# Kernel optimization log

Measured on AMD Instinct MI355X. Metric: run time of the kernel, lower is better.

The kernel has to match this reference:

```python
import jax, jax.numpy as jnp
import numpy as np


def setup_inputs() -> dict:
    key = jax.random.key(0)
    ks = jax.random.split(key, 7)
    N = 262144
    Ka, La = 8, 8
    Kb, Lb, Mb = 8, 8, 4
    Kc, Lc, Mc = 8, 8, 4
    return {
        "x": jax.random.normal(ks[0], (N, 2), dtype=jnp.float32),
        "a_real": 0.001 * jax.random.normal(ks[1], (Ka, La), dtype=jnp.float32),
        "a_imag": 0.001 * jax.random.normal(ks[2], (Ka, La), dtype=jnp.float32),
        "b_real": 0.001 * jax.random.normal(ks[3], (Kb, Lb, Mb), dtype=jnp.float32),
        "b_imag": 0.001 * jax.random.normal(ks[4], (Kb, Lb, Mb), dtype=jnp.float32),
        "c_real": 0.001 * jax.random.normal(ks[5], (Kc, Lc, Mc), dtype=jnp.float32),
        "c_imag": 0.001 * jax.random.normal(ks[6], (Kc, Lc, Mc), dtype=jnp.float32),
    }


def _gmp(x, a_real, a_imag, b_real, b_imag, c_real, c_imag):
    # x: (N,2) real I/Q -> complex signal (iq_handler equivalent)
    xc = (x[:, 0] + 1j * x[:, 1]).astype(jnp.complex64)
    a = (a_real + 1j * a_imag).astype(jnp.complex64)   # (Ka,La)
    b = (b_real + 1j * b_imag).astype(jnp.complex64)   # (Kb,Lb,Mb)
    c = (c_real + 1j * c_imag).astype(jnp.complex64)   # (Kc,Lc,Mc)
    N = xc.shape[0]
    Ka, La = a.shape
    Kb, Lb, Mb = b.shape
    Kc, Lc, Mc = c.shape
    n = jnp.arange(N)

    # ---- aligned term (a): delayed taps, power series in |x[n-l]| ----
    idx_La = jnp.clip(n[None, :] - jnp.arange(La)[:, None], 0, N - 1)   # (La,N)
    x_La = xc[idx_La]                                                   # (La,N)
    pow_a = jnp.abs(x_La)[..., None] ** jnp.arange(Ka, dtype=jnp.float32)  # (La,N,Ka)
    term_a = jnp.einsum('kl,ln,lnk->n', a, x_La, pow_a)

    # ---- lagging cross-term (b): envelope delayed by extra m >= 0 ----
    idx_Lb = jnp.clip(n[None, :] - jnp.arange(Lb)[:, None], 0, N - 1)   # (Lb,N)
    x_Lb = xc[idx_Lb]                                                   # (Lb,N)
    idx_Mb = jnp.clip(n[None, None, :] - jnp.arange(Lb)[:, None, None]
                      - jnp.arange(Mb)[None, :, None], 0, N - 1)        # (Lb,Mb,N)
    x_Mb = xc[idx_Mb]                                                   # (Lb,Mb,N)
    pow_b = jnp.abs(x_Mb)[..., None] ** jnp.arange(Kb, dtype=jnp.float32)  # (Lb,Mb,N,Kb)
    term_b = jnp.einsum('klm,ln,lmnk->n', b, x_Lb, pow_b)

    # ---- leading cross-term (c): envelope advanced by m >= 0 ----
    idx_Lc = jnp.clip(n[None, :] - jnp.arange(Lc)[:, None], 0, N - 1)   # (Lc,N)
    x_Lc = xc[idx_Lc]                                                   # (Lc,N)
    idx_Mc = jnp.clip(n[None, None, :] - jnp.arange(Lc)[:, None, None]
                      + jnp.arange(Mc)[None, :, None], 0, N - 1)        # (Lc,Mc,N)
    x_Mc = xc[idx_Mc]                                                   # (Lc,Mc,N)
    pow_c = jnp.abs(x_Mc)[..., None] ** jnp.arange(Kc, dtype=jnp.float32)  # (Lc,Mc,N,Kc)
    term_c = jnp.einsum('klm,ln,lmnk->n', c, x_Lc, pow_c)

    y = term_a + term_b + term_c                                        # (N,) complex
    return jnp.stack([y.real, y.imag], axis=-1)                         # back to I/Q (N,2)


def reference(x, a_real, a_imag, b_real, b_imag, c_real, c_imag):
    return _gmp(x, a_real, a_imag, b_real, b_imag, c_real, c_imag)
```

## Files before the change

kernel.cpp:

```cpp
#include <hip/hip_runtime.h>
#include <type_traits>

typedef float v2f __attribute__((ext_vector_type(2)));

template <typename T>
using cptr = T __attribute__((address_space(4)))*;

constexpr int BLOCK = 256;
constexpr int SPB = 128;
constexpr int HALO_LO = 10;
constexpr int HALO_HI = 3;
constexpr int SIG = SPB + HALO_LO + HALO_HI;

template<int I, int N, typename F>
__device__ __forceinline__ void unroll_for(F&& f) {
    if constexpr (I < N) {
        f(std::integral_constant<int, I>{});
        unroll_for<I + 1, N>(static_cast<F&&>(f));
    }
}

__global__ void prefold_kernel(
    const float* __restrict__ a_re, const float* __restrict__ a_im,
    const float* __restrict__ b_re, const float* __restrict__ b_im,
    const float* __restrict__ c_re, const float* __restrict__ c_im,
    float* __restrict__ w)
{
    int idx = threadIdx.x;
    if (idx >= 448) return;
    int l = idx / 56;
    int rem = idx - l * 56;
    int s = rem >> 3;
    int k = rem & 7;
    int akl = k * 8 + l;
    float re, im;
    if (s == 0) {
        re = a_re[akl] + b_re[akl * 4] + c_re[akl * 4];
        im = a_im[akl] + b_im[akl * 4] + c_im[akl * 4];
    } else if (s <= 3) {
        re = b_re[akl * 4 + s];
        im = b_im[akl * 4 + s];
    } else {
        re = c_re[akl * 4 + (s - 3)];
        im = c_im[akl * 4 + (s - 3)];
    }
    w[idx * 2]     = re;
    w[idx * 2 + 1] = im;
}

__global__ __launch_bounds__(BLOCK, 8) void gmp_kernel(
    const float* __restrict__ x,
    const float* __restrict__ wbuf,
    float* __restrict__ out, int N)
{
    __shared__ float2 sx[SIG];
    __shared__ float sab[SIG];
    __shared__ float2 part[4][SPB];

    const int t = threadIdx.x;
    const int n0 = blockIdx.x * SPB;

    const float2* x2 = (const float2*)x;
    if (t < SIG) {
        int g = n0 - HALO_LO + t;
        g = max(0, min(N - 1, g));
        float2 v = x2[g];
        sx[t] = v;
        sab[t] = __builtin_amdgcn_sqrtf(fmaf(v.x, v.x, v.y * v.y));
    }
    __syncthreads();

    const int s2 = t & 63;
    const int wv = __builtin_amdgcn_readfirstlane(t >> 6);
    auto cw = (cptr<const float>)(unsigned long long)(wbuf + wv * 224);

    const int rb = 2 * s2 + 6 - 2 * wv;
    float rv[9];
    unroll_for<0, 9>([&](auto I) { rv[I.value] = sab[rb + I.value]; });
    float xvr[3], xvi[3];
    unroll_for<0, 3>([&](auto I) {
        float2 v = sx[rb + 3 + I.value];
        xvr[I.value] = v.x;
        xvi[I.value] = v.y;
    });

    float y0r = 0.f, y0i = 0.f, y1r = 0.f, y1i = 0.f;

    unroll_for<0, 2>([&](auto LL) {
        constexpr int ll = LL.value;
        v2f S0 = {0.f, 0.f}, S1 = {0.f, 0.f};
        unroll_for<0, 7>([&](auto Sc) {
            constexpr int s = Sc.value;
            constexpr int d = (s == 0) ? 0 : ((s <= 3) ? -s : (s - 3));
            constexpr int off = ll * 112 + s * 16;
            float cre[8], cim[8];
            unroll_for<0, 8>([&](auto K) {
                cre[K.value] = cw[off + 2 * K.value];
                cim[K.value] = cw[off + 2 * K.value + 1];
            });
            const float r0 = rv[4 - ll + d];
            const float r1 = rv[5 - ll + d];
            const v2f rr0 = {r0, r0};
            const v2f rr1 = {r1, r1};
            v2f acc0 = {cre[7], cim[7]};
            v2f acc1 = acc0;
            unroll_for<0, 7>([&](auto Kc) {
                constexpr int k = 6 - Kc.value;
                const v2f wk = {cre[k], cim[k]};
                acc0 = __builtin_elementwise_fma(acc0, rr0, wk);
                acc1 = __builtin_elementwise_fma(acc1, rr1, wk);
            });
            S0 += acc0;
            S1 += acc1;
        });
        {
            const float xre = xvr[1 - ll], xim = xvi[1 - ll];
            y0r = fmaf(xre, S0.x, fmaf(-xim, S0.y, y0r));
            y0i = fmaf(xre, S0.y, fmaf( xim, S0.x, y0i));
        }
        {
            const float xre = xvr[2 - ll], xim = xvi[2 - ll];
            y1r = fmaf(xre, S1.x, fmaf(-xim, S1.y, y1r));
            y1i = fmaf(xre, S1.y, fmaf( xim, S1.x, y1i));
        }
    });

    part[wv][2 * s2]     = make_float2(y0r, y0i);
    part[wv][2 * s2 + 1] = make_float2(y1r, y1i);
    __syncthreads();

    if (t < SPB) {
        float2 p0 = part[0][t];
        float2 p1 = part[1][t];
        float2 p2 = part[2][t];
        float2 p3 = part[3][t];
        float2 r;
        r.x = (p0.x + p1.x) + (p2.x + p3.x);
        r.y = (p0.y + p1.y) + (p2.y + p3.y);
        const int n = n0 + t;
        if (n < N) ((float2*)out)[n] = r;
    }
}

extern "C" void kernel_launch(void* const* d_in, const int* in_sizes, int n_in,
                              void* d_out, int out_size, void* d_ws, size_t ws_size,
                              hipStream_t stream) {
    const float* x    = (const float*)d_in[0];
    const float* a_re = (const float*)d_in[1];
    const float* a_im = (const float*)d_in[2];
    const float* b_re = (const float*)d_in[3];
    const float* b_im = (const float*)d_in[4];
    const float* c_re = (const float*)d_in[5];
    const float* c_im = (const float*)d_in[6];
    float* out = (float*)d_out;
    float* w   = (float*)d_ws;

    int N = in_sizes[0] / 2;
    prefold_kernel<<<1, 448, 0, stream>>>(a_re, a_im, b_re, b_im, c_re, c_im, w);
    int grid = (N + SPB - 1) / SPB;
    gmp_kernel<<<grid, BLOCK, 0, stream>>>(x, w, out, N);
}
```

Baseline: 15.36 us.

## Fuse coefficient prefold into main kernel and stage weights in LDS

Removes the separate single-block prefold launch. Every block now folds the a/b/c coefficients itself into a shared-memory buffer, and the main loop reads the weights as float2 from LDS instead of through scalar constant-address loads. This drops one kernel launch and the dependency between the two kernels. In exchange, every block repeats the gather of about 1.3K coefficient floats, and the weight reads move from scalar registers and the SGPR path to vector LDS loads, which may add LDS pressure and VGPR use. The occupancy hint of 8 in launch_bounds is also removed.

Result: faster. 14.04 us (-8.6%).

```diff
diff --git a/kernel.cpp b/kernel.cpp
--- a/kernel.cpp
+++ b/kernel.cpp
@@ -2,9 +2,6 @@
 #include <type_traits>
 
 typedef float v2f __attribute__((ext_vector_type(2)));
-
-template <typename T>
-using cptr = T __attribute__((address_space(4)))*;
 
 constexpr int BLOCK = 256;
 constexpr int SPB = 128;
@@ -20,42 +17,17 @@
     }
 }
 
-__global__ void prefold_kernel(
+__global__ __launch_bounds__(BLOCK) void gmp_kernel(
+    const float* __restrict__ x,
     const float* __restrict__ a_re, const float* __restrict__ a_im,
     const float* __restrict__ b_re, const float* __restrict__ b_im,
     const float* __restrict__ c_re, const float* __restrict__ c_im,
-    float* __restrict__ w)
-{
-    int idx = threadIdx.x;
-    if (idx >= 448) return;
-    int l = idx / 56;
-    int rem = idx - l * 56;
-    int s = rem >> 3;
-    int k = rem & 7;
-    int akl = k * 8 + l;
-    float re, im;
-    if (s == 0) {
-        re = a_re[akl] + b_re[akl * 4] + c_re[akl * 4];
-        im = a_im[akl] + b_im[akl * 4] + c_im[akl * 4];
-    } else if (s <= 3) {
-        re = b_re[akl * 4 + s];
-        im = b_im[akl * 4 + s];
-    } else {
-        re = c_re[akl * 4 + (s - 3)];
-        im = c_im[akl * 4 + (s - 3)];
-    }
-    w[idx * 2]     = re;
-    w[idx * 2 + 1] = im;
-}
-
-__global__ __launch_bounds__(BLOCK, 8) void gmp_kernel(
-    const float* __restrict__ x,
-    const float* __restrict__ wbuf,
     float* __restrict__ out, int N)
 {
     __shared__ float2 sx[SIG];
     __shared__ float sab[SIG];
     __shared__ float2 part[4][SPB];
+    __shared__ __align__(16) float wlds[896];
 
     const int t = threadIdx.x;
     const int n0 = blockIdx.x * SPB;
@@ -68,11 +40,32 @@
         sx[t] = v;
         sab[t] = __builtin_amdgcn_sqrtf(fmaf(v.x, v.x, v.y * v.y));
     }
+
+    for (int idx = t; idx < 448; idx += BLOCK) {
+        int l = idx / 56;
+        int rem = idx - l * 56;
+        int s = rem >> 3;
+        int k = rem & 7;
+        int akl = k * 8 + l;
+        float re, im;
+        if (s == 0) {
+            re = a_re[akl] + b_re[akl * 4] + c_re[akl * 4];
+            im = a_im[akl] + b_im[akl * 4] + c_im[akl * 4];
+        } else if (s <= 3) {
+            re = b_re[akl * 4 + s];
+            im = b_im[akl * 4 + s];
+        } else {
+            re = c_re[akl * 4 + (s - 3)];
+            im = c_im[akl * 4 + (s - 3)];
+        }
+        wlds[idx * 2]     = re;
+        wlds[idx * 2 + 1] = im;
+    }
     __syncthreads();
 
     const int s2 = t & 63;
     const int wv = __builtin_amdgcn_readfirstlane(t >> 6);
-    auto cw = (cptr<const float>)(unsigned long long)(wbuf + wv * 224);
+    const float* cw = &wlds[wv * 224];
 
     const int rb = 2 * s2 + 6 - 2 * wv;
     float rv[9];
@@ -93,22 +86,20 @@
             constexpr int s = Sc.value;
             constexpr int d = (s == 0) ? 0 : ((s <= 3) ? -s : (s - 3));
             constexpr int off = ll * 112 + s * 16;
-            float cre[8], cim[8];
+            v2f wk[8];
             unroll_for<0, 8>([&](auto K) {
-                cre[K.value] = cw[off + 2 * K.value];
-                cim[K.value] = cw[off + 2 * K.value + 1];
+                wk[K.value] = *(const v2f*)&cw[off + 2 * K.value];
             });
             const float r0 = rv[4 - ll + d];
             const float r1 = rv[5 - ll + d];
             const v2f rr0 = {r0, r0};
             const v2f rr1 = {r1, r1};
-            v2f acc0 = {cre[7], cim[7]};
+            v2f acc0 = wk[7];
             v2f acc1 = acc0;
             unroll_for<0, 7>([&](auto Kc) {
                 constexpr int k = 6 - Kc.value;
-                const v2f wk = {cre[k], cim[k]};
-                acc0 = __builtin_elementwise_fma(acc0, rr0, wk);
-                acc1 = __builtin_elementwise_fma(acc1, rr1, wk);
+                acc0 = __builtin_elementwise_fma(acc0, rr0, wk[k]);
+                acc1 = __builtin_elementwise_fma(acc1, rr1, wk[k]);
             });
             S0 += acc0;
             S1 += acc1;
@@ -153,10 +144,9 @@
     const float* c_re = (const float*)d_in[5];
     const float* c_im = (const float*)d_in[6];
     float* out = (float*)d_out;
-    float* w   = (float*)d_ws;
 
     int N = in_sizes[0] / 2;
-    prefold_kernel<<<1, 448, 0, stream>>>(a_re, a_im, b_re, b_im, c_re, c_im, w);
     int grid = (N + SPB - 1) / SPB;
-    gmp_kernel<<<grid, BLOCK, 0, stream>>>(x, w, out, N);
+    gmp_kernel<<<grid, BLOCK, 0, stream>>>(x, a_re, a_im, b_re, b_im,
+                                           c_re, c_im, out, N);
 }
```
